# Performance work log

Measured on AMD Instinct MI355X. Metric: run time of the kernel, lower is better.

Reference implementation:

```python
import jax, jax.numpy as jnp
import numpy as np

STATE_LEN = 128
SEQ_LEN = 2048  # middle segment length; total T = SEQ_LEN + 2*STATE_LEN = 2304


def _l2norm(t):
    # matches torch F.normalize(p=2, dim=-1, eps=1e-12)
    n = jnp.sqrt(jnp.sum(t * t, axis=-1, keepdims=True))
    return t / jnp.maximum(n, 1e-12)


def setup_inputs() -> dict:
    key = jax.random.key(0)
    ks = jax.random.split(key, 8)
    B, D, H, dk, dv = 1, 1024, 16, 64, 64
    T = SEQ_LEN + 2 * STATE_LEN
    x = jax.random.normal(ks[0], (B, T, D), dtype=jnp.float32)
    w = lambda k, do: jax.random.normal(k, (H, D, do), dtype=jnp.float32) * 0.02
    return {
        "x": x,
        "Wq": w(ks[1], dk),
        "Wk": w(ks[2], dk),
        "Wv": w(ks[3], dv),
        "Wq_state": w(ks[4], dk),
        "Wk_state": w(ks[5], dk),
        "Wv_state": w(ks[6], dv),
        "scaling_factor": jnp.full((H,), 1.0 / np.sqrt(dk), dtype=jnp.float32),
    }


def reference(x, Wq, Wk, Wv, Wq_state, Wk_state, Wv_state, scaling_factor):
    sl, seq = STATE_LEN, SEQ_LEN
    # extract_state: [start_state | sequence | end_state]
    x0 = x[:, :sl]
    xm = x[:, sl:sl + seq]
    x1 = x[:, sl + seq:]

    proj = lambda t, W: jnp.einsum('bsd,hdk->bhsk', t, W)  # StackedLinear, no bias

    q = jnp.concatenate([_l2norm(proj(x0, Wq_state)), _l2norm(proj(xm, Wq)), _l2norm(proj(x1, Wq_state))], axis=2)
    k = jnp.concatenate([_l2norm(proj(x0, Wk_state)), _l2norm(proj(xm, Wk)), _l2norm(proj(x1, Wk_state))], axis=2)
    v = jnp.concatenate([_l2norm(proj(x0, Wv_state)), _l2norm(proj(xm, Wv)), _l2norm(proj(x1, Wv_state))], axis=2)

    T = q.shape[2]
    row = jnp.arange(T)[:, None]
    col = jnp.arange(T)[None, :]
    allowed = col <= row  # causal (tril, diagonal=0)
    # end-state rows may not attend to start-state cols (attn_bias[..., seq+sl:seq+2sl, :sl] = 0 before log)
    allowed = allowed & ~((row >= sl + seq) & (col < sl))
    mask = jnp.where(allowed, 0.0, -jnp.inf).astype(q.dtype)  # log of 0/1 tril

    # per-head learnable scale applied to q@k^T, then additive mask, softmax, @v
    scores = jnp.einsum('bhqd,bhkd->bhqk', q, k) * scaling_factor[None, :, None, None] + mask
    att = jax.nn.softmax(scores, axis=-1)
    return jnp.einsum('bhqk,bhkd->bhqd', att, v)
```

## Files before the change

### kernel.cpp

```cpp
#include <hip/hip_runtime.h>
#include <hip/hip_bf16.h>

#define T_TOT 2304
#define DDIM  1024
#define NH    16
#define DK    64
#define SLEN  128
#define SEQ   2048

typedef __bf16 bf16x8 __attribute__((ext_vector_type(8)));
typedef __bf16 bf16x4 __attribute__((ext_vector_type(4)));
typedef float  f32x4  __attribute__((ext_vector_type(4)));

__device__ __forceinline__ void async_copy16(const void* gsrc, void* ldst) {
  __builtin_amdgcn_global_load_lds(
      (const __attribute__((address_space(1))) void*)gsrc,
      (__attribute__((address_space(3))) void*)ldst, 16, 0, 0);
}

__global__ __launch_bounds__(256) void convert_kernel(
    const float* __restrict__ x,
    const float* __restrict__ Wq, const float* __restrict__ Wk,
    const float* __restrict__ Wv, const float* __restrict__ Wqs,
    const float* __restrict__ Wks, const float* __restrict__ Wvs,
    __bf16* __restrict__ xb, __bf16* __restrict__ Wt) {
  const int b = blockIdx.x;
  const int tid = threadIdx.x;
  if (b < 576) {
    const float4* xin = (const float4*)x;
#pragma unroll
    for (int it = 0; it < 4; ++it) {
      int idx4 = b * 1024 + it * 256 + tid;
      float4 v = xin[idx4];
      bf16x4 o;
      o[0] = (__bf16)v.x; o[1] = (__bf16)v.y; o[2] = (__bf16)v.z; o[3] = (__bf16)v.w;
      *(bf16x4*)(xb + (size_t)idx4 * 4) = o;
    }
    return;
  }
  __shared__ float tile[64 * 65];
  const int wb = b - 576;
  const int m  = wb >> 8;
  const int rem = wb & 255;
  const int h  = rem >> 4;
  const int dt = rem & 15;
  const int d0 = dt * 64;
  const float* Wsrc = (m == 0 ? Wq : m == 1 ? Wk : m == 2 ? Wv
                      : m == 3 ? Wqs : m == 4 ? Wks : Wvs) + (size_t)h * (DDIM * DK);
#pragma unroll
  for (int rr = 0; rr < 4; ++rr) {
    int drow = rr * 16 + (tid >> 4);
    int nc   = (tid & 15) * 4;
    float4 v = *(const float4*)(Wsrc + (size_t)(d0 + drow) * DK + nc);
    tile[(nc + 0) * 65 + drow] = v.x;
    tile[(nc + 1) * 65 + drow] = v.y;
    tile[(nc + 2) * 65 + drow] = v.z;
    tile[(nc + 3) * 65 + drow] = v.w;
  }
  __syncthreads();
  {
    int n  = tid >> 2;
    int rg = (tid & 3) * 16;
    __bf16* dst = Wt + (((size_t)(m * NH + h)) * DK + n) * DDIM + d0 + rg;
    bf16x8 o0, o1;
#pragma unroll
    for (int e = 0; e < 8; e++) o0[e] = (__bf16)tile[n * 65 + rg + e];
#pragma unroll
    for (int e = 0; e < 8; e++) o1[e] = (__bf16)tile[n * 65 + rg + 8 + e];
    *(bf16x8*)dst = o0;
    *(bf16x8*)(dst + 8) = o1;
  }
}

__global__ __launch_bounds__(256) void proj_kernel(
    const __bf16* __restrict__ xb, const __bf16* __restrict__ Wt,
    const float* __restrict__ scal,
    __bf16* __restrict__ qkv, __bf16* __restrict__ vt) {
  const int ntile = blockIdx.x;
  const int rt    = blockIdx.y;
  const int which = blockIdx.z;
  const int r0    = rt * 128;
  const int m     = (rt == 0 || rt == 17) ? which + 3 : which;

  __shared__ __bf16 Xs[128 * 64];
  __shared__ __bf16 Wsh[128 * 64];

  const int tid  = threadIdx.x;
  const int wave = tid >> 6, lane = tid & 63;
  const int quad = lane >> 4, lc = lane & 15;
  const int wr   = wave >> 1, wc = wave & 1;
  const int h    = ntile * 2 + wc;

  const __bf16* Wbase = Wt + ((size_t)m * NH) * (DK * DDIM) + (size_t)(ntile * 128) * DDIM;

  const f32x4 fz = {0.f, 0.f, 0.f, 0.f};
  f32x4 acc[4][4];
#pragma unroll
  for (int i = 0; i < 4; i++)
#pragma unroll
    for (int j = 0; j < 4; j++) acc[i][j] = fz;

  for (int k0 = 0; k0 < DDIM; k0 += 64) {
#pragma unroll
    for (int it = 0; it < 4; ++it) {
      int L = it * 256 + tid;
      int row = L >> 3, c = (L & 7) ^ ((L >> 3) & 7);
      async_copy16(xb + (size_t)(r0 + row) * DDIM + k0 + c * 8,
                   (char*)Xs + (size_t)(it * 256 + wave * 64) * 16);
    }
#pragma unroll
    for (int it = 0; it < 4; ++it) {
      int L = it * 256 + tid;
      int row = L >> 3, c = (L & 7) ^ ((L >> 3) & 7);
      async_copy16(Wbase + (size_t)row * DDIM + k0 + c * 8,
                   (char*)Wsh + (size_t)(it * 256 + wave * 64) * 16);
    }
    __syncthreads();
#pragma unroll
    for (int kk = 0; kk < 2; kk++) {
      bf16x8 afr[4], bfr[4];
#pragma unroll
      for (int i = 0; i < 4; i++) {
        int row = wr * 64 + i * 16 + lc;
        int ch  = (kk * 4 + quad) ^ (row & 7);
        afr[i] = *(const bf16x8*)(Xs + (row * 8 + ch) * 8);
      }
#pragma unroll
      for (int j = 0; j < 4; j++) {
        int row = wc * 64 + j * 16 + lc;
        int ch  = (kk * 4 + quad) ^ (row & 7);
        bfr[j] = *(const bf16x8*)(Wsh + (row * 8 + ch) * 8);
      }
#pragma unroll
      for (int i = 0; i < 4; i++)
#pragma unroll
        for (int j = 0; j < 4; j++)
          acc[i][j] = __builtin_amdgcn_mfma_f32_16x16x32_bf16(afr[i], bfr[j], acc[i][j], 0, 0, 0);
    }
    __syncthreads();
  }

  const float qscale = (which == 0) ? scal[h] * 1.44269504088896f : 1.0f;
  float inv4[4][4];
#pragma unroll
  for (int i = 0; i < 4; i++) {
#pragma unroll
    for (int r = 0; r < 4; r++) {
      float s = 0.f;
#pragma unroll
      for (int j = 0; j < 4; j++) { float v = acc[i][j][r]; s += v * v; }
#pragma unroll
      for (int off = 1; off < 16; off <<= 1) s += __shfl_xor(s, off, 64);
      inv4[i][r] = qscale / fmaxf(sqrtf(s), 1e-12f);
    }
  }
  if (which == 2) {
    __bf16* vtp = vt + (size_t)h * (DK * T_TOT);
#pragma unroll
    for (int i = 0; i < 4; i++) {
      int rowbase = r0 + wr * 64 + i * 16 + quad * 4;
#pragma unroll
      for (int j = 0; j < 4; j++) {
        bf16x4 o;
#pragma unroll
        for (int r = 0; r < 4; r++) o[r] = (__bf16)(acc[i][j][r] * inv4[i][r]);
        *(bf16x4*)(vtp + (size_t)(j * 16 + lc) * T_TOT + rowbase) = o;
      }
    }
  } else {
    __bf16* outp = qkv + ((size_t)(which * NH + h)) * ((size_t)T_TOT * DK);
#pragma unroll
    for (int i = 0; i < 4; i++)
#pragma unroll
      for (int r = 0; r < 4; r++) {
        int row = r0 + wr * 64 + i * 16 + quad * 4 + r;
#pragma unroll
        for (int j = 0; j < 4; j++)
          outp[(size_t)row * DK + j * 16 + lc] = (__bf16)(acc[i][j][r] * inv4[i][r]);
      }
  }
}

__global__ __launch_bounds__(256) void attn_kernel(
    const __bf16* __restrict__ qkv, const __bf16* __restrict__ vt,
    float* __restrict__ out) {
  const int b    = blockIdx.x;
  const int h    = b & 15;
  const int qg   = 35 - (b >> 4);
  const int q0b  = qg * 64;
  const int tid  = threadIdx.x;
  const int wave = tid >> 6, lane = tid & 63;
  const int quad = lane >> 4, lc = lane & 15;
  const int q0w  = q0b + wave * 16;

  const __bf16* qp = qkv + ((size_t)h) * ((size_t)T_TOT * DK);
  const __bf16* kp = qkv + ((size_t)(NH + h)) * ((size_t)T_TOT * DK);
  const __bf16* vp = vt + (size_t)h * (DK * T_TOT);

  __shared__ __bf16 Ks[2][128 * 64];
  __shared__ __bf16 Vs[2][64 * 128];
  __shared__ __bf16 Ps[4][16 * 128];

  bf16x8 qf[2];
#pragma unroll
  for (int kk = 0; kk < 2; kk++)
    qf[kk] = *(const bf16x8*)(qp + (size_t)(q0w + lc) * DK + kk * 32 + quad * 8);

  const f32x4 fz = {0.f, 0.f, 0.f, 0.f};
  f32x4 acc_o[4];
#pragma unroll
  for (int ct = 0; ct < 4; ct++) acc_o[ct] = fz;
  float l_part = 0.f;

  const int jstart = (q0b >= SLEN + SEQ) ? 1 : 0;
  const int jend   = q0b >> 7;

  auto stage = [&](int j, int bufi) {
    const __bf16* kT = kp + (size_t)j * 128 * DK;
#pragma unroll
    for (int it = 0; it < 4; ++it) {
      int L = it * 256 + tid;
      int row = L >> 3, c = (L & 7) ^ ((L >> 3) & 7);
      async_copy16(kT + row * DK + c * 8,
                   (char*)&Ks[bufi][0] + (size_t)(it * 256 + wave * 64) * 16);
    }
#pragma unroll
    for (int it = 0; it < 4; ++it) {
      int L = it * 256 + tid;
      int d = L >> 4, c = (L & 15) ^ ((L >> 4) & 15);
      async_copy16(vp + (size_t)d * T_TOT + j * 128 + c * 8,
                   (char*)&Vs[bufi][0] + (size_t)(it * 256 + wave * 64) * 16);
    }
  };

  stage(jstart, 0);
  int cur = 0;

  for (int j = jstart; j <= jend; ++j) {
    __syncthreads();
    if (j < jend) stage(j + 1, cur ^ 1);

    const int c0 = j * 128;
    const bool diag = (j == jend);
    const int ctmax = diag ? ((q0b & 64) ? 7 : 3) : 7;

    f32x4 s[8];
#pragma unroll
    for (int ct = 0; ct < 8; ct++) {
      s[ct] = fz;
      if (ct <= ctmax) {
#pragma unroll
        for (int kk = 0; kk < 2; kk++) {
          int row = ct * 16 + lc;
          bf16x8 kA = *(const bf16x8*)(&Ks[cur][(row * 8 + ((kk * 4 + quad) ^ (row & 7))) * 8]);
          s[ct] = __builtin_amdgcn_mfma_f32_16x16x32_bf16(kA, qf[kk], s[ct], 0, 0, 0);
        }
      }
    }

#pragma unroll
    for (int ct = 0; ct < 8; ct++) {
      if (ct > ctmax) break;
      if (diag) {
#pragma unroll
        for (int r = 0; r < 4; r++)
          if ((c0 + ct * 16 + quad * 4 + r) > (q0w + lc)) s[ct][r] = -__builtin_inff();
      }
      bf16x4 pb;
#pragma unroll
      for (int r = 0; r < 4; r++) {
        float pe = exp2f(s[ct][r]);
        l_part += pe;
        pb[r] = (__bf16)pe;
      }
      int cc = ct * 2 + (quad >> 1);
      int el = lc * 128 + ((cc ^ (lc & 15)) * 8) + (quad & 1) * 4;
      *(bf16x4*)(&Ps[wave][el]) = pb;
    }

    const int kqmax = diag ? ((q0b & 64) ? 3 : 1) : 3;
#pragma unroll
    for (int kq = 0; kq < 4; kq++) {
      if (kq > kqmax) break;
      int cc = kq * 4 + quad;
      bf16x8 pB = *(const bf16x8*)(&Ps[wave][lc * 128 + ((cc ^ (lc & 15)) * 8)]);
#pragma unroll
      for (int ct = 0; ct < 4; ct++) {
        int d = ct * 16 + lc;
        bf16x8 vA = *(const bf16x8*)(&Vs[cur][(d * 16 + (cc ^ (d & 15))) * 8]);
        acc_o[ct] = __builtin_amdgcn_mfma_f32_16x16x32_bf16(vA, pB, acc_o[ct], 0, 0, 0);
      }
    }
    cur ^= 1;
  }

  float l_i = l_part;
  l_i += __shfl_xor(l_i, 16, 64);
  l_i += __shfl_xor(l_i, 32, 64);
  float invl = 1.0f / l_i;
#pragma unroll
  for (int ct = 0; ct < 4; ct++) {
    f32x4 o;
#pragma unroll
    for (int r = 0; r < 4; r++) o[r] = acc_o[ct][r] * invl;
    *(f32x4*)(&out[((size_t)h * T_TOT + q0w + lc) * DK + ct * 16 + quad * 4]) = o;
  }
}

extern "C" void kernel_launch(void* const* d_in, const int* in_sizes, int n_in,
                              void* d_out, int out_size, void* d_ws, size_t ws_size,
                              hipStream_t stream) {
  const float* x    = (const float*)d_in[0];
  const float* Wq   = (const float*)d_in[1];
  const float* Wk   = (const float*)d_in[2];
  const float* Wv   = (const float*)d_in[3];
  const float* Wqs  = (const float*)d_in[4];
  const float* Wks  = (const float*)d_in[5];
  const float* Wvs  = (const float*)d_in[6];
  const float* scal = (const float*)d_in[7];
  float* out = (float*)d_out;

  char* ws = (char*)d_ws;
  size_t off = 0;
  __bf16* xb  = (__bf16*)(ws + off); off += (size_t)T_TOT * DDIM * 2;
  __bf16* Wt  = (__bf16*)(ws + off); off += (size_t)6 * NH * DK * DDIM * 2;
  __bf16* qkv = (__bf16*)(ws + off); off += (size_t)2 * NH * T_TOT * DK * 2;
  __bf16* vt  = (__bf16*)(ws + off);

  convert_kernel<<<2112, 256, 0, stream>>>(x, Wq, Wk, Wv, Wqs, Wks, Wvs, xb, Wt);
  proj_kernel<<<dim3(8, 18, 3), 256, 0, stream>>>(xb, Wt, scal, qkv, vt);
  attn_kernel<<<dim3(576), 256, 0, stream>>>(qkv, vt, out);
}
```

Before: 155.8 us.

## Restructure attention to 64-key tiles shared across waves with 32x32 MFMA for PV

The attention kernel now processes 64-key blocks instead of 128. Each wave computes scores for 16 keys against all 64 queries of the block, writes probabilities into a shared P tile, and then does PV with 32x32x16 MFMA on a 32x32 output quadrant. Row sums are reduced across waves through LDS. It also adds a lighter LDS barrier, halves the shared memory footprint and sets launch bounds for 3 blocks per SM. This should raise occupancy and cut redundant masking on the diagonal, at the cost of an extra barrier per iteration and a cross-wave reduction.

Result: no change. 155.7 us (-0.0%).

```diff
diff --git a/kernel.cpp b/kernel.cpp
--- a/kernel.cpp
+++ b/kernel.cpp
@@ -11,11 +11,16 @@
 typedef __bf16 bf16x8 __attribute__((ext_vector_type(8)));
 typedef __bf16 bf16x4 __attribute__((ext_vector_type(4)));
 typedef float  f32x4  __attribute__((ext_vector_type(4)));
+typedef float  f32x16 __attribute__((ext_vector_type(16)));
 
 __device__ __forceinline__ void async_copy16(const void* gsrc, void* ldst) {
   __builtin_amdgcn_global_load_lds(
       (const __attribute__((address_space(1))) void*)gsrc,
       (__attribute__((address_space(3))) void*)ldst, 16, 0, 0);
+}
+
+__device__ __forceinline__ void lds_barrier() {
+  __asm__ volatile("s_waitcnt lgkmcnt(0)\n\ts_barrier" ::: "memory");
 }
 
 __global__ __launch_bounds__(256) void convert_kernel(
@@ -181,7 +186,7 @@
   }
 }
 
-__global__ __launch_bounds__(256) void attn_kernel(
+__global__ __launch_bounds__(256, 3) void attn_kernel(
     const __bf16* __restrict__ qkv, const __bf16* __restrict__ vt,
     float* __restrict__ out) {
   const int b    = blockIdx.x;
@@ -191,119 +196,124 @@
   const int tid  = threadIdx.x;
   const int wave = tid >> 6, lane = tid & 63;
   const int quad = lane >> 4, lc = lane & 15;
-  const int q0w  = q0b + wave * 16;
+  const int l32  = lane & 31, hi = lane >> 5;
 
   const __bf16* qp = qkv + ((size_t)h) * ((size_t)T_TOT * DK);
   const __bf16* kp = qkv + ((size_t)(NH + h)) * ((size_t)T_TOT * DK);
   const __bf16* vp = vt + (size_t)h * (DK * T_TOT);
 
-  __shared__ __bf16 Ks[2][128 * 64];
-  __shared__ __bf16 Vs[2][64 * 128];
-  __shared__ __bf16 Ps[4][16 * 128];
-
-  bf16x8 qf[2];
-#pragma unroll
-  for (int kk = 0; kk < 2; kk++)
-    qf[kk] = *(const bf16x8*)(qp + (size_t)(q0w + lc) * DK + kk * 32 + quad * 8);
-
-  const f32x4 fz = {0.f, 0.f, 0.f, 0.f};
-  f32x4 acc_o[4];
-#pragma unroll
-  for (int ct = 0; ct < 4; ct++) acc_o[ct] = fz;
-  float l_part = 0.f;
-
-  const int jstart = (q0b >= SLEN + SEQ) ? 1 : 0;
-  const int jend   = q0b >> 7;
+  __shared__ __bf16 Ks[2][64 * 64];
+  __shared__ __bf16 Vs[2][64 * 64];
+  __shared__ __bf16 Ps[64 * 64];
+  __shared__ float  lred[4][64];
+
+  bf16x8 qf[4][2];
+#pragma unroll
+  for (int qt = 0; qt < 4; qt++)
+#pragma unroll
+    for (int kk = 0; kk < 2; kk++)
+      qf[qt][kk] = *(const bf16x8*)(qp + (size_t)(q0b + qt * 16 + lc) * DK + kk * 32 + quad * 8);
+
+  f32x16 acc_o;
+#pragma unroll
+  for (int e = 0; e < 16; e++) acc_o[e] = 0.f;
+  float lp[4] = {0.f, 0.f, 0.f, 0.f};
+
+  const int jstart = (q0b >= SLEN + SEQ) ? 2 : 0;
+  const int jend   = qg;
 
   auto stage = [&](int j, int bufi) {
-    const __bf16* kT = kp + (size_t)j * 128 * DK;
-#pragma unroll
-    for (int it = 0; it < 4; ++it) {
+    const __bf16* kT = kp + (size_t)j * 64 * DK;
+#pragma unroll
+    for (int it = 0; it < 2; ++it) {
       int L = it * 256 + tid;
       int row = L >> 3, c = (L & 7) ^ ((L >> 3) & 7);
-      async_copy16(kT + row * DK + c * 8,
+      async_copy16(kT + (size_t)row * DK + c * 8,
                    (char*)&Ks[bufi][0] + (size_t)(it * 256 + wave * 64) * 16);
     }
 #pragma unroll
-    for (int it = 0; it < 4; ++it) {
+    for (int it = 0; it < 2; ++it) {
       int L = it * 256 + tid;
-      int d = L >> 4, c = (L & 15) ^ ((L >> 4) & 15);
-      async_copy16(vp + (size_t)d * T_TOT + j * 128 + c * 8,
+      int d = L >> 3, c = (L & 7) ^ ((L >> 3) & 7);
+      async_copy16(vp + (size_t)d * T_TOT + j * 64 + c * 8,
                    (char*)&Vs[bufi][0] + (size_t)(it * 256 + wave * 64) * 16);
     }
   };
 
   stage(jstart, 0);
   int cur = 0;
+
+  const int d0 = (wave >> 1) * 32;
+  const int q0 = (wave & 1) * 32;
 
   for (int j = jstart; j <= jend; ++j) {
     __syncthreads();
     if (j < jend) stage(j + 1, cur ^ 1);
 
-    const int c0 = j * 128;
     const bool diag = (j == jend);
-    const int ctmax = diag ? ((q0b & 64) ? 7 : 3) : 7;
-
-    f32x4 s[8];
-#pragma unroll
-    for (int ct = 0; ct < 8; ct++) {
-      s[ct] = fz;
-      if (ct <= ctmax) {
-#pragma unroll
-        for (int kk = 0; kk < 2; kk++) {
-          int row = ct * 16 + lc;
-          bf16x8 kA = *(const bf16x8*)(&Ks[cur][(row * 8 + ((kk * 4 + quad) ^ (row & 7))) * 8]);
-          s[ct] = __builtin_amdgcn_mfma_f32_16x16x32_bf16(kA, qf[kk], s[ct], 0, 0, 0);
-        }
-      }
-    }
-
-#pragma unroll
-    for (int ct = 0; ct < 8; ct++) {
-      if (ct > ctmax) break;
+
+    bf16x8 kA[2];
+#pragma unroll
+    for (int kk = 0; kk < 2; kk++) {
+      int row = wave * 16 + lc;
+      kA[kk] = *(const bf16x8*)(&Ks[cur][(row * 8 + ((kk * 4 + quad) ^ (lc & 7))) * 8]);
+    }
+    f32x4 s[4];
+#pragma unroll
+    for (int qt = 0; qt < 4; qt++) {
+      s[qt] = (f32x4){0.f, 0.f, 0.f, 0.f};
+#pragma unroll
+      for (int kk = 0; kk < 2; kk++)
+        s[qt] = __builtin_amdgcn_mfma_f32_16x16x32_bf16(kA[kk], qf[qt][kk], s[qt], 0, 0, 0);
+    }
+
+#pragma unroll
+    for (int qt = 0; qt < 4; qt++) {
       if (diag) {
 #pragma unroll
         for (int r = 0; r < 4; r++)
-          if ((c0 + ct * 16 + quad * 4 + r) > (q0w + lc)) s[ct][r] = -__builtin_inff();
+          if ((wave * 16 + quad * 4 + r) > (qt * 16 + lc)) s[qt][r] = -__builtin_inff();
       }
       bf16x4 pb;
 #pragma unroll
       for (int r = 0; r < 4; r++) {
-        float pe = exp2f(s[ct][r]);
-        l_part += pe;
+        float pe = exp2f(s[qt][r]);
+        lp[qt] += pe;
         pb[r] = (__bf16)pe;
       }
-      int cc = ct * 2 + (quad >> 1);
-      int el = lc * 128 + ((cc ^ (lc & 15)) * 8) + (quad & 1) * 4;
-      *(bf16x4*)(&Ps[wave][el]) = pb;
-    }
-
-    const int kqmax = diag ? ((q0b & 64) ? 3 : 1) : 3;
-#pragma unroll
-    for (int kq = 0; kq < 4; kq++) {
-      if (kq > kqmax) break;
-      int cc = kq * 4 + quad;
-      bf16x8 pB = *(const bf16x8*)(&Ps[wave][lc * 128 + ((cc ^ (lc & 15)) * 8)]);
-#pragma unroll
-      for (int ct = 0; ct < 4; ct++) {
-        int d = ct * 16 + lc;
-        bf16x8 vA = *(const bf16x8*)(&Vs[cur][(d * 16 + (cc ^ (d & 15))) * 8]);
-        acc_o[ct] = __builtin_amdgcn_mfma_f32_16x16x32_bf16(vA, pB, acc_o[ct], 0, 0, 0);
-      }
+      int el = (qt * 16 + lc) * 64 + (((wave * 2 + (quad >> 1)) ^ (lc & 7)) * 8) + (quad & 1) * 4;
+      *(bf16x4*)(&Ps[el]) = pb;
+    }
+
+    lds_barrier();
+
+#pragma unroll
+    for (int ks = 0; ks < 4; ks++) {
+      int ch = (ks * 2 + hi) ^ (l32 & 7);
+      bf16x8 vA = *(const bf16x8*)(&Vs[cur][((d0 + l32) * 8 + ch) * 8]);
+      bf16x8 pB = *(const bf16x8*)(&Ps[((q0 + l32) * 8 + ch) * 8]);
+      acc_o = __builtin_amdgcn_mfma_f32_32x32x16_bf16(vA, pB, acc_o, 0, 0, 0);
     }
     cur ^= 1;
   }
 
-  float l_i = l_part;
-  l_i += __shfl_xor(l_i, 16, 64);
-  l_i += __shfl_xor(l_i, 32, 64);
-  float invl = 1.0f / l_i;
-#pragma unroll
-  for (int ct = 0; ct < 4; ct++) {
+#pragma unroll
+  for (int qt = 0; qt < 4; qt++) {
+    lp[qt] += __shfl_xor(lp[qt], 16, 64);
+    lp[qt] += __shfl_xor(lp[qt], 32, 64);
+  }
+  lred[wave][quad * 16 + lc] = lp[quad];
+  __syncthreads();
+  float lsum = lred[0][q0 + l32] + lred[1][q0 + l32] + lred[2][q0 + l32] + lred[3][q0 + l32];
+  float invl = 1.0f / lsum;
+
+  const size_t rowbase = ((size_t)h * T_TOT + q0b + q0 + l32) * DK;
+#pragma unroll
+  for (int g = 0; g < 4; g++) {
     f32x4 o;
 #pragma unroll
-    for (int r = 0; r < 4; r++) o[r] = acc_o[ct][r] * invl;
-    *(f32x4*)(&out[((size_t)h * T_TOT + q0w + lc) * DK + ct * 16 + quad * 4]) = o;
+    for (int t = 0; t < 4; t++) o[t] = acc_o[g * 4 + t] * invl;
+    *(f32x4*)(&out[rowbase + d0 + 4 * hi + 8 * g]) = o;
   }
 }
 
```
